# Optimization experiments

Measured on AMD Instinct MI355X. Metric: run time of the kernel, lower is better.

## Reference

```python
import jax, jax.numpy as jnp
import numpy as np

NUM_HEADS = 16
ROPE_THETA = 10000.0


def apply_rope(x, pos):
    # x: [b, h, s, d_head]; rotates consecutive pairs (2i, 2i+1)
    d = x.shape[-1]
    inv_freq = ROPE_THETA ** (-jnp.arange(0, d, 2, dtype=x.dtype) / d)  # [d/2]
    ang = pos.astype(x.dtype)[:, None] * inv_freq[None, :]              # [s, d/2]
    cos, sin = jnp.cos(ang), jnp.sin(ang)
    x1, x2 = x[..., 0::2], x[..., 1::2]
    rot = jnp.stack([x1 * cos - x2 * sin, x1 * sin + x2 * cos], axis=-1)
    return rot.reshape(x.shape)


def setup_inputs() -> dict:
    key = jax.random.key(0)
    k1, k2, k3 = jax.random.split(key, 3)
    d_model = 1024
    x = jax.random.normal(k1, (4, 2048, d_model), dtype=jnp.float32)
    wqkv = jax.random.normal(k2, (3 * d_model, d_model), dtype=jnp.float32) * 0.02
    wout = jax.random.normal(k3, (d_model, d_model), dtype=jnp.float32) * 0.02
    return {"x": x, "wqkv": wqkv, "wout": wout}


def reference(x, wqkv, wout):
    b, s, d_model = x.shape
    h = NUM_HEADS
    d_head = d_model // h

    qkv = jnp.einsum("bsd,ed->bse", x, wqkv)              # [b, s, 3*d_model]
    q, k, v = jnp.split(qkv, 3, axis=-1)

    def split_heads(t):  # [b, s, d_model] -> [b, h, s, d_head]
        return t.reshape(b, s, h, d_head).transpose(0, 2, 1, 3)

    q, k, v = split_heads(q), split_heads(k), split_heads(v)

    pos = jnp.arange(s)
    q = apply_rope(q, pos)
    k = apply_rope(k, pos)

    scale = 1.0 / jnp.sqrt(jnp.asarray(d_head, dtype=x.dtype))
    scores = jnp.einsum("bhqd,bhkd->bhqk", q, k) * scale   # [b, h, s, s]
    causal = jnp.tril(jnp.ones((s, s), dtype=bool))
    scores = jnp.where(causal, scores, jnp.finfo(scores.dtype).min)
    attn = jax.nn.softmax(scores, axis=-1)
    y = jnp.einsum("bhqk,bhkd->bhqd", attn, v)             # [b, h, s, d_head]
    y = y.transpose(0, 2, 1, 3).reshape(b, s, d_model)
    return jnp.einsum("bsd,ed->bse", y, wout)
```

## Files before the change

kernel.cpp:

```cpp
#include <hip/hip_runtime.h>
#include <stdint.h>

typedef uint16_t u16;
typedef __bf16 bf16x8 __attribute__((ext_vector_type(8)));
typedef float   f32x4 __attribute__((ext_vector_type(4)));
typedef uint16_t u16x2 __attribute__((ext_vector_type(2)));
typedef uint16_t u16x4 __attribute__((ext_vector_type(4)));
typedef uint16_t u16x8 __attribute__((ext_vector_type(8)));
typedef float   f32x4g __attribute__((ext_vector_type(4)));

#define DEV __device__ __forceinline__

DEV u16 f2bf(float f) {
  __bf16 h = (__bf16)f;
  return __builtin_bit_cast(u16, h);
}
DEV float bf2f(u16 u) {
  union { uint32_t u; float f; } v; v.u = ((uint32_t)u) << 16;
  return v.f;
}
DEV float exp2fast(float x) {
  float r; asm("v_exp_f32 %0, %1" : "=v"(r) : "v"(x)); return r;
}

DEV void gload_lds16(const u16* g, u16* l) {
  __builtin_amdgcn_global_load_lds((const __attribute__((address_space(1))) void*)g,
                                   (__attribute__((address_space(3))) void*)l,
                                   16, 0, 0);
}

__global__ void sctab_kernel(float2* __restrict__ tab) {
  const int idx = blockIdx.x * 256 + threadIdx.x;
  const int s = idx >> 5, i = idx & 31;
  const float invf = (float)exp2(-2.0 * (double)i / 64.0 * 13.287712379549449);
  float sn, cs;
  sincosf((float)s * invf, &sn, &cs);
  tab[idx] = make_float2(cs, sn);
}

__global__ void cvt3_kernel(const float* __restrict__ a, u16* __restrict__ da,
                            const float* __restrict__ b, u16* __restrict__ db,
                            const float* __restrict__ c, u16* __restrict__ dc) {
  int i = blockIdx.x * 256 + threadIdx.x;
  const float* s; u16* d; int off;
  if (i < 2097152)      { s = a; d = da; off = i; }
  else if (i < 2883584) { s = b; d = db; off = i - 2097152; }
  else                  { s = c; d = dc; off = i - 2883584; }
  f32x4g v = ((const f32x4g*)s)[off];
  u16 tmp[4] = {f2bf(v[0]), f2bf(v[1]), f2bf(v[2]), f2bf(v[3])};
  *(uint64_t*)(d + (size_t)off * 4) = *(const uint64_t*)tmp;
}

__global__ __launch_bounds__(256) void gemm_qkv(const u16* __restrict__ A,
                                                const u16* __restrict__ B,
                                                const float2* __restrict__ tab,
                                                u16* __restrict__ Qh,
                                                u16* __restrict__ Kh,
                                                u16* __restrict__ Vt) {
  constexpr int K = 1024;
  constexpr int BK = 32;
  __shared__ __align__(16) u16 As[2][128 * BK];
  __shared__ __align__(16) u16 Bs[2][128 * BK];
  const int t = threadIdx.x;
  const int w = t >> 6, l = t & 63;
  const int l4 = l >> 4, l15 = l & 15;

  const int nbx = gridDim.x;
  const int nwg = gridDim.x * gridDim.y;
  const int orig = blockIdx.y * nbx + blockIdx.x;
  const int wgid = (orig & 7) * (nwg >> 3) + (orig >> 3);
  const int bm = (wgid / nbx) * 128, bn = (wgid % nbx) * 128;

  const int wr = (w >> 1) * 64, wc = (w & 1) * 64;

  const int srow = w * 32 + (l >> 2);
  const int scol = (l & 3) * 8;
  const u16* gA = A + (size_t)(bm + srow) * K + scol;
  const u16* gB = B + (size_t)(bn + srow) * K + scol;

  f32x4 acc[4][4];
#pragma unroll
  for (int m = 0; m < 4; ++m)
#pragma unroll
    for (int n = 0; n < 4; ++n) acc[m][n] = f32x4{0.f, 0.f, 0.f, 0.f};

  const int nkt = K / BK;

  auto stage = [&](int kt, int buf) {
    const u16* a0 = gA + (size_t)kt * BK;
    const u16* b0 = gB + (size_t)kt * BK;
    gload_lds16(a0,                  &As[buf][(w * 32) * BK]);
    gload_lds16(a0 + (size_t)16 * K, &As[buf][(w * 32 + 16) * BK]);
    gload_lds16(b0,                  &Bs[buf][(w * 32) * BK]);
    gload_lds16(b0 + (size_t)16 * K, &Bs[buf][(w * 32 + 16) * BK]);
  };

  stage(0, 0);
  __syncthreads();
  for (int kt = 0; kt < nkt; ++kt) {
    const int buf = kt & 1;
    if (kt + 1 < nkt) stage(kt + 1, buf ^ 1);
    bf16x8 af[4], bfr[4];
#pragma unroll
    for (int m = 0; m < 4; ++m) af[m]  = *(const bf16x8*)&As[buf][(wr + m * 16 + l15) * BK + l4 * 8];
#pragma unroll
    for (int n = 0; n < 4; ++n) bfr[n] = *(const bf16x8*)&Bs[buf][(wc + n * 16 + l15) * BK + l4 * 8];
#pragma unroll
    for (int m = 0; m < 4; ++m)
#pragma unroll
      for (int n = 0; n < 4; ++n)
        acc[m][n] = __builtin_amdgcn_mfma_f32_16x16x32_bf16(af[m], bfr[n], acc[m][n], 0, 0, 0);
    __syncthreads();
  }

  const int part = bn >> 10;
  const int ccbase = (bn & 1023) + wc;
  if (part == 2) {
#pragma unroll
    for (int m = 0; m < 4; ++m) {
      const int row0 = bm + wr + m * 16 + l4 * 4;
      const int bb = row0 >> 11, s0 = row0 & 2047;
#pragma unroll
      for (int n = 0; n < 4; ++n) {
        const int cc = ccbase + n * 16 + l15;
        const int hh = cc >> 6, dd = cc & 63;
        u16x4 pk = {f2bf(acc[m][n][0]), f2bf(acc[m][n][1]), f2bf(acc[m][n][2]), f2bf(acc[m][n][3])};
        *(u16x4*)(Vt + ((size_t)(bb * 16 + hh) * 64 + dd) * 2048 + s0) = pk;
      }
    }
  } else {
    const float qs = (part == 0) ? 0.18033688011112042f : 1.0f;
    u16* const Out = (part == 0) ? Qh : Kh;
#pragma unroll
    for (int m = 0; m < 4; ++m) {
      const int row0 = bm + wr + m * 16 + l4 * 4;
      const int bb = row0 >> 11, s0 = row0 & 2047;
#pragma unroll
      for (int n = 0; n < 4; ++n) {
        const int cc = ccbase + n * 16 + l15;
        const int hh = cc >> 6, dd = cc & 63;
        const int fi = dd >> 1;
        const float sgn = (dd & 1) ? 1.f : -1.f;
        u16* outp = Out + ((size_t)(bb * 16 + hh) * 2048 + s0) * 64 + dd;
#pragma unroll
        for (int r = 0; r < 4; ++r) {
          const float a = acc[m][n][r];
          const float other = __shfl_xor(a, 1);
          const float2 cs2 = tab[(size_t)(s0 + r) * 32 + fi];
          outp[(size_t)r * 64] = f2bf((a * cs2.x + other * sgn * cs2.y) * qs);
        }
      }
    }
  }
}

template<bool OUT_BF16>
__global__ __launch_bounds__(256) void gemm_bt(const u16* __restrict__ A,
                                               const u16* __restrict__ B,
                                               void* __restrict__ Cv,
                                               int M, int N, int K) {
  constexpr int BK = 32;
  __shared__ __align__(16) u16 As[2][128 * BK];
  __shared__ __align__(16) u16 Bs[2][128 * BK];
  const int t = threadIdx.x;
  const int w = t >> 6, l = t & 63;
  const int l4 = l >> 4, l15 = l & 15;

  const int nbx = gridDim.x;
  const int nwg = gridDim.x * gridDim.y;
  const int orig = blockIdx.y * nbx + blockIdx.x;
  const int wgid = (orig & 7) * (nwg >> 3) + (orig >> 3);
  const int bm = (wgid / nbx) * 128, bn = (wgid % nbx) * 128;

  const int wr = (w >> 1) * 64, wc = (w & 1) * 64;

  const int srow = w * 32 + (l >> 2);
  const int scol = (l & 3) * 8;
  const u16* gA = A + (size_t)(bm + srow) * K + scol;
  const u16* gB = B + (size_t)(bn + srow) * K + scol;

  f32x4 acc[4][4];
#pragma unroll
  for (int m = 0; m < 4; ++m)
#pragma unroll
    for (int n = 0; n < 4; ++n) acc[m][n] = f32x4{0.f, 0.f, 0.f, 0.f};

  const int nkt = K / BK;

  auto stage = [&](int kt, int buf) {
    const u16* a0 = gA + (size_t)kt * BK;
    const u16* b0 = gB + (size_t)kt * BK;
    gload_lds16(a0,                  &As[buf][(w * 32) * BK]);
    gload_lds16(a0 + (size_t)16 * K, &As[buf][(w * 32 + 16) * BK]);
    gload_lds16(b0,                  &Bs[buf][(w * 32) * BK]);
    gload_lds16(b0 + (size_t)16 * K, &Bs[buf][(w * 32 + 16) * BK]);
  };

  stage(0, 0);
  __syncthreads();
  for (int kt = 0; kt < nkt; ++kt) {
    const int buf = kt & 1;
    if (kt + 1 < nkt) stage(kt + 1, buf ^ 1);
    bf16x8 af[4], bfr[4];
#pragma unroll
    for (int m = 0; m < 4; ++m) af[m]  = *(const bf16x8*)&As[buf][(wr + m * 16 + l15) * BK + l4 * 8];
#pragma unroll
    for (int n = 0; n < 4; ++n) bfr[n] = *(const bf16x8*)&Bs[buf][(wc + n * 16 + l15) * BK + l4 * 8];
#pragma unroll
    for (int m = 0; m < 4; ++m)
#pragma unroll
      for (int n = 0; n < 4; ++n)
        acc[m][n] = __builtin_amdgcn_mfma_f32_16x16x32_bf16(af[m], bfr[n], acc[m][n], 0, 0, 0);
    __syncthreads();
  }

#pragma unroll
  for (int m = 0; m < 4; ++m) {
    const int row0 = bm + wr + m * 16 + l4 * 4;
#pragma unroll
    for (int n = 0; n < 4; ++n) {
      const int col = bn + wc + n * 16 + l15;
#pragma unroll
      for (int r = 0; r < 4; ++r) {
        if (OUT_BF16) ((u16*)Cv)[(size_t)(row0 + r) * N + col] = f2bf(acc[m][n][r]);
        else          ((float*)Cv)[(size_t)(row0 + r) * N + col] = acc[m][n][r];
      }
    }
  }
}

__global__ __launch_bounds__(256) void attn_kernel(const u16* __restrict__ Qh,
                                                   const u16* __restrict__ Kh,
                                                   const u16* __restrict__ Vt,
                                                   u16* __restrict__ Y) {
  __shared__ __align__(16) u16 Ks[64][72];
  __shared__ __align__(16) u16 Vs[64][72];
  __shared__ __align__(16) u16 Ps[4][32][72];
  const int t = threadIdx.x, w = t >> 6, l = t & 63;
  const int l4 = l >> 4, l15 = l & 15;
  const int bid = blockIdx.x;
  const int p   = (bid >> 3) & 15;
  const int bh  = ((bid >> 7) << 3) | (bid & 7);
  const int b = bh >> 4, h = bh & 15;
  const int qb0 = p * 64 + w * 16;
  const int qb1 = (31 - p) * 64 + w * 16;
  const u16* Qb = Qh + (size_t)bh * 2048 * 64;
  const u16* Kb = Kh + (size_t)bh * 2048 * 64;
  const u16* Vb = Vt + (size_t)bh * 64 * 2048;

  bf16x8 qf[2][2];
  {
    const int qb[2] = {qb0, qb1};
#pragma unroll
    for (int m = 0; m < 2; ++m)
#pragma unroll
      for (int ks = 0; ks < 2; ++ks)
        qf[m][ks] = *(const bf16x8*)(Qb + (size_t)(qb[m] + l15) * 64 + ks * 32 + l4 * 8);
  }

  f32x4 o[2][4];
#pragma unroll
  for (int m = 0; m < 2; ++m)
#pragma unroll
    for (int nd = 0; nd < 4; ++nd) o[m][nd] = f32x4{0.f, 0.f, 0.f, 0.f};
  float lsum[2] = {0.f, 0.f};

  const int sr = t >> 3;
  const int scol = (t & 7) * 8;
  const int nkv = 32 - p;

  u16x8 rk0 = *(const u16x8*)(Kb + (size_t)sr * 64 + scol);
  u16x8 rk1 = *(const u16x8*)(Kb + (size_t)(sr + 32) * 64 + scol);
  u16x8 rv0 = *(const u16x8*)(Vb + (size_t)sr * 2048 + scol);
  u16x8 rv1 = *(const u16x8*)(Vb + (size_t)(sr + 32) * 2048 + scol);

  for (int kv = 0; kv < nkv; ++kv) {
    const int kv0 = kv * 64;
    __syncthreads();
    *(u16x8*)&Ks[sr][scol]      = rk0;
    *(u16x8*)&Ks[sr + 32][scol] = rk1;
    *(u16x8*)&Vs[sr][scol]      = rv0;
    *(u16x8*)&Vs[sr + 32][scol] = rv1;
    __syncthreads();
    if (kv + 1 < nkv) {
      const int n0 = kv0 + 64;
      rk0 = *(const u16x8*)(Kb + (size_t)(n0 + sr) * 64 + scol);
      rk1 = *(const u16x8*)(Kb + (size_t)(n0 + sr + 32) * 64 + scol);
      rv0 = *(const u16x8*)(Vb + (size_t)sr * 2048 + n0 + scol);
      rv1 = *(const u16x8*)(Vb + (size_t)(sr + 32) * 2048 + n0 + scol);
    }

    auto SCORE = [&](int m, int qbm) {
      f32x4 sfr[4];
      __builtin_amdgcn_s_setprio(1);
#pragma unroll
      for (int n = 0; n < 4; ++n) {
        bf16x8 kf0 = *(const bf16x8*)&Ks[n * 16 + l15][l4 * 8];
        bf16x8 kf1 = *(const bf16x8*)&Ks[n * 16 + l15][32 + l4 * 8];
        f32x4 a = f32x4{0.f, 0.f, 0.f, 0.f};
        a = __builtin_amdgcn_mfma_f32_16x16x32_bf16(kf0, qf[m][0], a, 0, 0, 0);
        a = __builtin_amdgcn_mfma_f32_16x16x32_bf16(kf1, qf[m][1], a, 0, 0, 0);
        sfr[n] = a;
      }
      __builtin_amdgcn_s_setprio(0);
      if (kv0 + 63 > qbm) {
        const int q = qbm + l15;
#pragma unroll
        for (int n = 0; n < 4; ++n)
#pragma unroll
          for (int r = 0; r < 4; ++r)
            if (kv0 + n * 16 + l4 * 4 + r > q) sfr[n][r] = -1e30f;
      }
      float rs = 0.f;
#pragma unroll
      for (int n = 0; n < 4; ++n) {
#pragma unroll
        for (int r = 0; r < 4; ++r) {
          const float pv = exp2fast(sfr[n][r]);
          sfr[n][r] = pv; rs += pv;
        }
        u16x4 pk = {f2bf(sfr[n][0]), f2bf(sfr[n][1]), f2bf(sfr[n][2]), f2bf(sfr[n][3])};
        *(u16x4*)&Ps[w][m * 16 + l15][n * 16 + l4 * 4] = pk;
      }
      lsum[m] += rs;
    };

    SCORE(1, qb1);
    if (kv <= p) SCORE(0, qb0);

    bf16x8 vfr[4][2];
#pragma unroll
    for (int nd = 0; nd < 4; ++nd) {
      vfr[nd][0] = *(const bf16x8*)&Vs[nd * 16 + l15][l4 * 8];
      vfr[nd][1] = *(const bf16x8*)&Vs[nd * 16 + l15][32 + l4 * 8];
    }

    auto PV = [&](int m) {
      bf16x8 pf0 = *(const bf16x8*)&Ps[w][m * 16 + l15][l4 * 8];
      bf16x8 pf1 = *(const bf16x8*)&Ps[w][m * 16 + l15][32 + l4 * 8];
      __builtin_amdgcn_s_setprio(1);
#pragma unroll
      for (int nd = 0; nd < 4; ++nd) {
        o[m][nd] = __builtin_amdgcn_mfma_f32_16x16x32_bf16(pf0, vfr[nd][0], o[m][nd], 0, 0, 0);
        o[m][nd] = __builtin_amdgcn_mfma_f32_16x16x32_bf16(pf1, vfr[nd][1], o[m][nd], 0, 0, 0);
      }
      __builtin_amdgcn_s_setprio(0);
    };
    PV(1);
    if (kv <= p) PV(0);
  }

  const int qb[2] = {qb0, qb1};
#pragma unroll
  for (int m = 0; m < 2; ++m) {
    lsum[m] += __shfl_xor(lsum[m], 16);
    lsum[m] += __shfl_xor(lsum[m], 32);
    const float li = 1.0f / lsum[m];
    float lb[4];
#pragma unroll
    for (int r = 0; r < 4; ++r) lb[r] = __shfl(li, (l & 48) | (l4 * 4 + r));
#pragma unroll
    for (int r = 0; r < 4; ++r) {
      const size_t row = (size_t)b * 2048 + qb[m] + l4 * 4 + r;
#pragma unroll
      for (int nd = 0; nd < 4; ++nd)
        Y[row * 1024 + h * 64 + nd * 16 + l15] = f2bf(o[m][nd][r] * lb[r]);
    }
  }
}

extern "C" void kernel_launch(void* const* d_in, const int* in_sizes, int n_in,
                              void* d_out, int out_size, void* d_ws, size_t ws_size,
                              hipStream_t stream) {
  const float* x    = (const float*)d_in[0];
  const float* wqkv = (const float*)d_in[1];
  const float* wout = (const float*)d_in[2];
  float* out = (float*)d_out;
  char* ws = (char*)d_ws;

  u16* x_bf    = (u16*)(ws);
  u16* Y       = x_bf;
  u16* wqkv_bf = (u16*)(ws + 16777216);
  u16* wout_bf = (u16*)(ws + 23068672);
  float2* tab  = (float2*)(ws + 25165824);
  u16* Qh      = (u16*)(ws + 75497472);
  u16* Kh      = (u16*)(ws + 92274688);
  u16* Vt      = (u16*)(ws + 109051904);

  sctab_kernel<<<256, 256, 0, stream>>>(tab);
  cvt3_kernel<<<12288, 256, 0, stream>>>(x, x_bf, wqkv, wqkv_bf, wout, wout_bf);
  gemm_qkv<<<dim3(24, 64), 256, 0, stream>>>(x_bf, wqkv_bf, tab, Qh, Kh, Vt);
  attn_kernel<<<1024, 256, 0, stream>>>(Qh, Kh, Vt, Y);
  gemm_bt<false><<<dim3(8, 64), 256, 0, stream>>>(Y, wout_bf, out, 8192, 1024, 1024);
}
```

Before: 204.4 us.

## Replace paired causal query tiles with one tile per block ordered longest-first

The attention kernel previously gave each block two query tiles (p and 31-p) so every block had a balanced amount of causal work. It now gives each block a single 64-row query tile and doubles the grid to 2048 blocks. Block IDs are ordered so the tiles with the most KV blocks launch first, and the occupancy hint is raised to 5 blocks per CU. This trades the pairing's load balance and its K/V reuse across two tiles for more parallelism, lower register use and higher occupancy. It also means each K/V tile is loaded roughly twice as often.

```diff
diff --git a/kernel.cpp b/kernel.cpp
--- a/kernel.cpp
+++ b/kernel.cpp
@@ -229,45 +229,37 @@
   }
 }
 
-__global__ __launch_bounds__(256) void attn_kernel(const u16* __restrict__ Qh,
-                                                   const u16* __restrict__ Kh,
-                                                   const u16* __restrict__ Vt,
-                                                   u16* __restrict__ Y) {
+__global__ __launch_bounds__(256, 5) void attn_kernel(const u16* __restrict__ Qh,
+                                                      const u16* __restrict__ Kh,
+                                                      const u16* __restrict__ Vt,
+                                                      u16* __restrict__ Y) {
   __shared__ __align__(16) u16 Ks[64][72];
   __shared__ __align__(16) u16 Vs[64][72];
-  __shared__ __align__(16) u16 Ps[4][32][72];
+  __shared__ __align__(16) u16 Ps[4][16][72];
   const int t = threadIdx.x, w = t >> 6, l = t & 63;
   const int l4 = l >> 4, l15 = l & 15;
   const int bid = blockIdx.x;
-  const int p   = (bid >> 3) & 15;
-  const int bh  = ((bid >> 7) << 3) | (bid & 7);
+  const int s   = 31 - (bid >> 6);
+  const int bh  = bid & 63;
   const int b = bh >> 4, h = bh & 15;
-  const int qb0 = p * 64 + w * 16;
-  const int qb1 = (31 - p) * 64 + w * 16;
+  const int q0 = s * 64 + w * 16;
   const u16* Qb = Qh + (size_t)bh * 2048 * 64;
   const u16* Kb = Kh + (size_t)bh * 2048 * 64;
   const u16* Vb = Vt + (size_t)bh * 64 * 2048;
 
-  bf16x8 qf[2][2];
-  {
-    const int qb[2] = {qb0, qb1};
-#pragma unroll
-    for (int m = 0; m < 2; ++m)
-#pragma unroll
-      for (int ks = 0; ks < 2; ++ks)
-        qf[m][ks] = *(const bf16x8*)(Qb + (size_t)(qb[m] + l15) * 64 + ks * 32 + l4 * 8);
-  }
-
-  f32x4 o[2][4];
-#pragma unroll
-  for (int m = 0; m < 2; ++m)
-#pragma unroll
-    for (int nd = 0; nd < 4; ++nd) o[m][nd] = f32x4{0.f, 0.f, 0.f, 0.f};
-  float lsum[2] = {0.f, 0.f};
+  bf16x8 qf[2];
+#pragma unroll
+  for (int ks = 0; ks < 2; ++ks)
+    qf[ks] = *(const bf16x8*)(Qb + (size_t)(q0 + l15) * 64 + ks * 32 + l4 * 8);
+
+  f32x4 o[4];
+#pragma unroll
+  for (int nd = 0; nd < 4; ++nd) o[nd] = f32x4{0.f, 0.f, 0.f, 0.f};
+  float lsum = 0.f;
 
   const int sr = t >> 3;
   const int scol = (t & 7) * 8;
-  const int nkv = 32 - p;
+  const int nkv = s + 1;
 
   u16x8 rk0 = *(const u16x8*)(Kb + (size_t)sr * 64 + scol);
   u16x8 rk1 = *(const u16x8*)(Kb + (size_t)(sr + 32) * 64 + scol);
@@ -290,43 +282,38 @@
       rv1 = *(const u16x8*)(Vb + (size_t)(sr + 32) * 2048 + n0 + scol);
     }
 
-    auto SCORE = [&](int m, int qbm) {
-      f32x4 sfr[4];
-      __builtin_amdgcn_s_setprio(1);
-#pragma unroll
-      for (int n = 0; n < 4; ++n) {
-        bf16x8 kf0 = *(const bf16x8*)&Ks[n * 16 + l15][l4 * 8];
-        bf16x8 kf1 = *(const bf16x8*)&Ks[n * 16 + l15][32 + l4 * 8];
-        f32x4 a = f32x4{0.f, 0.f, 0.f, 0.f};
-        a = __builtin_amdgcn_mfma_f32_16x16x32_bf16(kf0, qf[m][0], a, 0, 0, 0);
-        a = __builtin_amdgcn_mfma_f32_16x16x32_bf16(kf1, qf[m][1], a, 0, 0, 0);
-        sfr[n] = a;
+    f32x4 sfr[4];
+    __builtin_amdgcn_s_setprio(1);
+#pragma unroll
+    for (int n = 0; n < 4; ++n) {
+      bf16x8 kf0 = *(const bf16x8*)&Ks[n * 16 + l15][l4 * 8];
+      bf16x8 kf1 = *(const bf16x8*)&Ks[n * 16 + l15][32 + l4 * 8];
+      f32x4 a = f32x4{0.f, 0.f, 0.f, 0.f};
+      a = __builtin_amdgcn_mfma_f32_16x16x32_bf16(kf0, qf[0], a, 0, 0, 0);
+      a = __builtin_amdgcn_mfma_f32_16x16x32_bf16(kf1, qf[1], a, 0, 0, 0);
+      sfr[n] = a;
+    }
+    __builtin_amdgcn_s_setprio(0);
+    if (kv == s) {
+      const int q = q0 + l15;
+#pragma unroll
+      for (int n = 0; n < 4; ++n)
+#pragma unroll
+        for (int r = 0; r < 4; ++r)
+          if (kv0 + n * 16 + l4 * 4 + r > q) sfr[n][r] = -1e30f;
+    }
+    float rs = 0.f;
+#pragma unroll
+    for (int n = 0; n < 4; ++n) {
+#pragma unroll
+      for (int r = 0; r < 4; ++r) {
+        const float pv = exp2fast(sfr[n][r]);
+        sfr[n][r] = pv; rs += pv;
       }
-      __builtin_amdgcn_s_setprio(0);
-      if (kv0 + 63 > qbm) {
-        const int q = qbm + l15;
-#pragma unroll
-        for (int n = 0; n < 4; ++n)
-#pragma unroll
-          for (int r = 0; r < 4; ++r)
-            if (kv0 + n * 16 + l4 * 4 + r > q) sfr[n][r] = -1e30f;
-      }
-      float rs = 0.f;
-#pragma unroll
-      for (int n = 0; n < 4; ++n) {
-#pragma unroll
-        for (int r = 0; r < 4; ++r) {
-          const float pv = exp2fast(sfr[n][r]);
-          sfr[n][r] = pv; rs += pv;
-        }
-        u16x4 pk = {f2bf(sfr[n][0]), f2bf(sfr[n][1]), f2bf(sfr[n][2]), f2bf(sfr[n][3])};
-        *(u16x4*)&Ps[w][m * 16 + l15][n * 16 + l4 * 4] = pk;
-      }
-      lsum[m] += rs;
-    };
-
-    SCORE(1, qb1);
-    if (kv <= p) SCORE(0, qb0);
+      u16x4 pk = {f2bf(sfr[n][0]), f2bf(sfr[n][1]), f2bf(sfr[n][2]), f2bf(sfr[n][3])};
+      *(u16x4*)&Ps[w][l15][n * 16 + l4 * 4] = pk;
+    }
+    lsum += rs;
 
     bf16x8 vfr[4][2];
 #pragma unroll
@@ -334,38 +321,29 @@
       vfr[nd][0] = *(const bf16x8*)&Vs[nd * 16 + l15][l4 * 8];
       vfr[nd][1] = *(const bf16x8*)&Vs[nd * 16 + l15][32 + l4 * 8];
     }
-
-    auto PV = [&](int m) {
-      bf16x8 pf0 = *(const bf16x8*)&Ps[w][m * 16 + l15][l4 * 8];
-      bf16x8 pf1 = *(const bf16x8*)&Ps[w][m * 16 + l15][32 + l4 * 8];
-      __builtin_amdgcn_s_setprio(1);
-#pragma unroll
-      for (int nd = 0; nd < 4; ++nd) {
-        o[m][nd] = __builtin_amdgcn_mfma_f32_16x16x32_bf16(pf0, vfr[nd][0], o[m][nd], 0, 0, 0);
-        o[m][nd] = __builtin_amdgcn_mfma_f32_16x16x32_bf16(pf1, vfr[nd][1], o[m][nd], 0, 0, 0);
-      }
-      __builtin_amdgcn_s_setprio(0);
-    };
-    PV(1);
-    if (kv <= p) PV(0);
-  }
-
-  const int qb[2] = {qb0, qb1};
-#pragma unroll
-  for (int m = 0; m < 2; ++m) {
-    lsum[m] += __shfl_xor(lsum[m], 16);
-    lsum[m] += __shfl_xor(lsum[m], 32);
-    const float li = 1.0f / lsum[m];
-    float lb[4];
-#pragma unroll
-    for (int r = 0; r < 4; ++r) lb[r] = __shfl(li, (l & 48) | (l4 * 4 + r));
-#pragma unroll
-    for (int r = 0; r < 4; ++r) {
-      const size_t row = (size_t)b * 2048 + qb[m] + l4 * 4 + r;
-#pragma unroll
-      for (int nd = 0; nd < 4; ++nd)
-        Y[row * 1024 + h * 64 + nd * 16 + l15] = f2bf(o[m][nd][r] * lb[r]);
-    }
+    bf16x8 pf0 = *(const bf16x8*)&Ps[w][l15][l4 * 8];
+    bf16x8 pf1 = *(const bf16x8*)&Ps[w][l15][32 + l4 * 8];
+    __builtin_amdgcn_s_setprio(1);
+#pragma unroll
+    for (int nd = 0; nd < 4; ++nd) {
+      o[nd] = __builtin_amdgcn_mfma_f32_16x16x32_bf16(pf0, vfr[nd][0], o[nd], 0, 0, 0);
+      o[nd] = __builtin_amdgcn_mfma_f32_16x16x32_bf16(pf1, vfr[nd][1], o[nd], 0, 0, 0);
+    }
+    __builtin_amdgcn_s_setprio(0);
+  }
+
+  lsum += __shfl_xor(lsum, 16);
+  lsum += __shfl_xor(lsum, 32);
+  const float li = 1.0f / lsum;
+  float lb[4];
+#pragma unroll
+  for (int r = 0; r < 4; ++r) lb[r] = __shfl(li, (l & 48) | (l4 * 4 + r));
+#pragma unroll
+  for (int r = 0; r < 4; ++r) {
+    const size_t row = (size_t)b * 2048 + q0 + l4 * 4 + r;
+#pragma unroll
+    for (int nd = 0; nd < 4; ++nd)
+      Y[row * 1024 + h * 64 + nd * 16 + l15] = f2bf(o[nd][r] * lb[r]);
   }
 }
 
@@ -390,6 +368,6 @@
   sctab_kernel<<<256, 256, 0, stream>>>(tab);
   cvt3_kernel<<<12288, 256, 0, stream>>>(x, x_bf, wqkv, wqkv_bf, wout, wout_bf);
   gemm_qkv<<<dim3(24, 64), 256, 0, stream>>>(x_bf, wqkv_bf, tab, Qh, Kh, Vt);
-  attn_kernel<<<1024, 256, 0, stream>>>(Qh, Kh, Vt, Y);
+  attn_kernel<<<2048, 256, 0, stream>>>(Qh, Kh, Vt, Y);
   gemm_bt<false><<<dim3(8, 64), 256, 0, stream>>>(Y, wout_bf, out, 8192, 1024, 1024);
 }
```

After: 204.6 us. About the same (+0.1%).
